# Optimization experiments

Measured on AMD Instinct MI355X. Metric: run time of the kernel, lower is better.

The kernel has to match this reference:

```python
import jax, jax.numpy as jnp
import numpy as np

B, P, CV = 2, 1024, 768
V, DNB, K = 50000, 300, 3
H = 768  # max(512, v_dim)
TOTAL_IN = CV + K * DNB + K  # include_scores=True
EPS = 1e-12


def setup_inputs() -> dict:
    key = jax.random.key(0)
    ks = jax.random.split(key, 7)
    v_seq = jax.random.normal(ks[0], (B, P, CV), dtype=jnp.float32)
    T = jax.random.normal(ks[1], (V, CV), dtype=jnp.float32)
    T_clip = T / jnp.linalg.norm(T, axis=-1, keepdims=True)  # bank rows are L2-normalized
    nb_vecs = jax.random.normal(ks[2], (V, DNB), dtype=jnp.float32)
    W1 = jax.random.normal(ks[3], (TOTAL_IN, H), dtype=jnp.float32) * (1.0 / np.sqrt(TOTAL_IN))
    b1 = jnp.zeros((H,), dtype=jnp.float32)
    W2 = jax.random.normal(ks[4], (H, CV), dtype=jnp.float32) * (1.0 / np.sqrt(H))
    b2 = jnp.zeros((CV,), dtype=jnp.float32)
    return {"v_seq": v_seq, "T_clip": T_clip, "nb_vecs": nb_vecs,
            "W1": W1, "b1": b1, "W2": W2, "b2": b2}


def _layer_norm(x, eps=1e-5):
    mu = jnp.mean(x, axis=-1, keepdims=True)
    var = jnp.var(x, axis=-1, keepdims=True)
    return (x - mu) * jax.lax.rsqrt(var + eps)


def reference(v_seq, T_clip, nb_vecs, W1, b1, W2, b2):
    # --- retrieve (no_grad in original) ---
    q = v_seq / jnp.maximum(jnp.linalg.norm(v_seq, axis=-1, keepdims=True), EPS)
    S = jnp.einsum('bpc,vc->bpv', q, T_clip)            # (B,P,V) cosine sims
    val, idx = jax.lax.top_k(S, K)                       # (B,P,K) each
    nb_sel = nb_vecs[idx]                                # gather -> (B,P,K,DNB)
    # --- fuse_concat ---
    nb_flat = nb_sel.reshape(B, P, K * DNB)
    combined = jnp.concatenate([v_seq, nb_flat, val], axis=-1)  # (B,P,TOTAL_IN)
    h = jax.nn.gelu(combined @ W1 + b1, approximate=False)      # nn.GELU default = erf
    fused = h @ W2 + b2                                          # dropout inactive (eval)
    return _layer_norm(fused)                                    # F.layer_norm, no affine
```

## Files before the change

### kernel.cpp

```cpp
#include <hip/hip_runtime.h>
#include <hip/hip_bf16.h>

typedef unsigned short u16;
typedef unsigned int u32;
typedef __attribute__((ext_vector_type(4))) unsigned short u16x4;
typedef __attribute__((ext_vector_type(8))) unsigned short u16x8;
typedef __attribute__((ext_vector_type(8))) short bf16x8;
typedef __attribute__((ext_vector_type(4))) float f32x4;

#define ROWS 2048
#define CV 768
#define VOCAB 50000
#define NPAD 50176
#define NTILES 196
#define NSEG 392
#define NSEGP 392
#define DNB 300
#define TOTAL_IN 1671
#define KPAD1 1696
#define HD 768
#define NT 12

__device__ __forceinline__ u16 f2bf(float f) {
  union { __hip_bfloat16 h; u16 u; } x;
  x.h = __float2bfloat16(f);
  return x.u;
}

__device__ __forceinline__ u16 bfkey(u16 u) {
  return (u & 0x8000) ? (u16)~u : (u16)(u | 0x8000);
}

__device__ __forceinline__ void gload16(const u16* g, const u16* l) {
  __builtin_amdgcn_global_load_lds(
      (const __attribute__((address_space(1))) void*)g,
      (__attribute__((address_space(3))) void*)l, 16, 0, 0);
}

__device__ __forceinline__ float block_sum256(float v, float* ws) {
#pragma unroll
  for (int off = 32; off > 0; off >>= 1) v += __shfl_xor(v, off, 64);
  int tid = threadIdx.x;
  if ((tid & 63) == 0) ws[tid >> 6] = v;
  __syncthreads();
  float s = ws[0] + ws[1] + ws[2] + ws[3];
  __syncthreads();
  return s;
}

__global__ __launch_bounds__(256) void normalize_kernel(
    const float* __restrict__ v_seq, float* __restrict__ rinv, u16* __restrict__ q16) {
  __shared__ float ws[4];
  int row = blockIdx.x, tid = threadIdx.x;
  const float* x = v_seq + (size_t)row * CV;
  float x0 = x[tid], x1 = x[tid + 256], x2 = x[tid + 512];
  float s = block_sum256(x0 * x0 + x1 * x1 + x2 * x2, ws);
  float denom = fmaxf(sqrtf(s), 1e-12f);
  float inv = 1.0f / denom;
  u16* qb = q16 + (size_t)row * CV;
  qb[tid] = f2bf(x0 * inv); qb[tid + 256] = f2bf(x1 * inv); qb[tid + 512] = f2bf(x2 * inv);
  if (tid == 0) rinv[row] = inv;
}

__global__ __launch_bounds__(256) void cvt_bf16_kernel(
    const float* __restrict__ src, u16* __restrict__ dst, int n4) {
  int i = blockIdx.x * 256 + threadIdx.x;
  int stride = gridDim.x * 256;
  for (; i < n4; i += stride) {
    float4 v = reinterpret_cast<const float4*>(src)[i];
    u16x4 o = {f2bf(v.x), f2bf(v.y), f2bf(v.z), f2bf(v.w)};
    reinterpret_cast<u16x4*>(dst)[i] = o;
  }
}

__global__ __launch_bounds__(256) void transpose_cvt_kernel(
    const float* __restrict__ src, u16* __restrict__ dst, int Ksrc, int ldk, int N) {
  __shared__ float tile[32][33];
  int tx = threadIdx.x & 31, ty = threadIdx.x >> 5;
  int kb = blockIdx.x * 32, nb = blockIdx.y * 32;
#pragma unroll
  for (int i = 0; i < 4; ++i) {
    int k = kb + ty + i * 8, n = nb + tx;
    tile[ty + i * 8][tx] = (k < Ksrc) ? src[(size_t)k * N + n] : 0.f;
  }
  __syncthreads();
#pragma unroll
  for (int i = 0; i < 4; ++i) {
    int n = nb + ty + i * 8, k = kb + tx;
    dst[(size_t)n * ldk + k] = f2bf(tile[tx][ty + i * 8]);
  }
}

__global__ __launch_bounds__(512, 2) void score_gemm_256(
    const u16* __restrict__ q16, const u16* __restrict__ T16,
    u16* __restrict__ S16, u16* __restrict__ segmax) {
  __shared__ __align__(16) u16 lds[65536];
  __shared__ float smx[256][4];

  int tid = threadIdx.x;
  int w = tid >> 6, lane = tid & 63;
  int wr = w >> 2, wc = w & 3;
  int l15 = lane & 15, l4 = lane >> 4;

  int bid = blockIdx.x;
  int wg = (bid & 7) * NTILES + (bid >> 3);
  int mtile = wg & 7, ntile = wg >> 3;
  int m0 = mtile * 256, n0 = ntile * 256;

  int t8 = tid >> 3;
  int jcol = (((tid & 7) ^ (t8 & 7)) << 3);
  int rowA = m0 + t8;
  int rowB0 = n0 + t8;        rowB0 = rowB0 > (VOCAB - 1) ? (VOCAB - 1) : rowB0;
  int rowB1 = n0 + 64 + t8;   rowB1 = rowB1 > (VOCAB - 1) ? (VOCAB - 1) : rowB1;
  int rowB2 = n0 + 128 + t8;  rowB2 = rowB2 > (VOCAB - 1) ? (VOCAB - 1) : rowB2;
  int rowB3 = n0 + 192 + t8;  rowB3 = rowB3 > (VOCAB - 1) ? (VOCAB - 1) : rowB3;
  int w512 = w * 512;

  int xorv = (l15 & 7) << 4;
  int l416 = l4 << 4;
  int c0 = ((l416) ^ xorv) >> 1;
  int c1 = ((64 + l416) ^ xorv) >> 1;
  int aro = (wr * 128 + l15) * 64;
  int bro = 16384 + (wc * 64 + l15) * 64;

  f32x4 acc[8][4];
#pragma unroll
  for (int i = 0; i < 8; ++i)
#pragma unroll
    for (int j = 0; j < 4; ++j) acc[i][j] = {0.f, 0.f, 0.f, 0.f};

  bf16x8 af[2][4], bfr[2][4];

#define STAGE_A(R0) gload16(q16 + (size_t)(rowA + (R0)) * CV + ktn + jcol, \
                            &lds[nbase + (R0) * 64 + w512])
#define STAGE_B0() gload16(T16 + (size_t)rowB0 * CV + ktn + jcol, &lds[nbase + 16384 + w512])
#define STAGE_B1() gload16(T16 + (size_t)rowB1 * CV + ktn + jcol, &lds[nbase + 16384 + 4096 + w512])
#define STAGE_B2() gload16(T16 + (size_t)rowB2 * CV + ktn + jcol, &lds[nbase + 16384 + 8192 + w512])
#define STAGE_B3() gload16(T16 + (size_t)rowB3 * CV + ktn + jcol, &lds[nbase + 16384 + 12288 + w512])

#define LDA4(MIB)                                                           \
  _Pragma("unroll") for (int ks = 0; ks < 2; ++ks)                          \
  _Pragma("unroll") for (int mi = 0; mi < 4; ++mi)                          \
    af[ks][mi] = *reinterpret_cast<const bf16x8*>(                          \
        &lds[cbase + aro + ((MIB) + mi) * 1024 + (ks ? c1 : c0)]);

#define LDB2(NIB)                                                           \
  _Pragma("unroll") for (int ks = 0; ks < 2; ++ks)                          \
  _Pragma("unroll") for (int ni = 0; ni < 2; ++ni)                          \
    bfr[ks][(NIB) + ni] = *reinterpret_cast<const bf16x8*>(                 \
        &lds[cbase + bro + ((NIB) + ni) * 1024 + (ks ? c1 : c0)]);

#define MFMAQ(MIB, NIB)                                                     \
  _Pragma("unroll") for (int mi = 0; mi < 4; ++mi)                          \
  _Pragma("unroll") for (int ni = 0; ni < 2; ++ni) {                        \
    acc[(MIB) + mi][(NIB) + ni] = __builtin_amdgcn_mfma_f32_16x16x32_bf16(  \
        af[0][mi], bfr[0][(NIB) + ni], acc[(MIB) + mi][(NIB) + ni], 0, 0, 0); \
    acc[(MIB) + mi][(NIB) + ni] = __builtin_amdgcn_mfma_f32_16x16x32_bf16(  \
        af[1][mi], bfr[1][(NIB) + ni], acc[(MIB) + mi][(NIB) + ni], 0, 0, 0); \
  }

  {
    int nbase = 0, ktn = 0;
    STAGE_B0(); STAGE_B1(); STAGE_B2(); STAGE_B3();
    STAGE_A(0); STAGE_A(128); STAGE_A(64); STAGE_A(192);
  }

  for (int t = 0; t < NT; ++t) {
    int cb = t & 1;
    int cbase = cb * 32768;
    int nbase = cbase ^ 32768;
    int ktn = ((t + 1 < NT) ? (t + 1) : t) * 64;

    asm volatile("s_waitcnt vmcnt(2)" ::: "memory");
    __builtin_amdgcn_s_barrier();

    LDA4(0)
    LDB2(0)
    STAGE_B0(); STAGE_B1();
    __builtin_amdgcn_s_barrier();
    __builtin_amdgcn_s_setprio(1);
    MFMAQ(0, 0)
    __builtin_amdgcn_s_setprio(0);
    __builtin_amdgcn_s_barrier();

    LDB2(2)
    STAGE_B2(); STAGE_B3();
    __builtin_amdgcn_s_barrier();
    __builtin_amdgcn_s_setprio(1);
    MFMAQ(0, 2)
    __builtin_amdgcn_s_setprio(0);
    asm volatile("s_waitcnt vmcnt(4)" ::: "memory");
    __builtin_amdgcn_s_barrier();

    LDA4(4)
    STAGE_A(0); STAGE_A(128);
    __builtin_amdgcn_s_barrier();
    __builtin_amdgcn_s_setprio(1);
    MFMAQ(4, 0)
    __builtin_amdgcn_s_setprio(0);
    __builtin_amdgcn_s_barrier();

    STAGE_A(64); STAGE_A(192);
    __builtin_amdgcn_s_setprio(1);
    MFMAQ(4, 2)
    __builtin_amdgcn_s_setprio(0);
  }
  asm volatile("s_waitcnt vmcnt(0)" ::: "memory");
  __builtin_amdgcn_s_barrier();

#pragma unroll
  for (int mi = 0; mi < 8; ++mi)
#pragma unroll
    for (int ni = 0; ni < 4; ++ni) {
      int gr = m0 + wr * 128 + mi * 16 + l4 * 4;
      int gc = n0 + wc * 64 + ni * 16 + l15;
#pragma unroll
      for (int r = 0; r < 4; ++r)
        S16[(size_t)(gr + r) * NPAD + gc] = f2bf(acc[mi][ni][r]);
    }

#pragma unroll
  for (int mi = 0; mi < 8; ++mi)
#pragma unroll
    for (int r = 0; r < 4; ++r) {
      float v = -3e38f;
#pragma unroll
      for (int ni = 0; ni < 4; ++ni) {
        bool ok = (n0 + wc * 64 + ni * 16 + l15) < VOCAB;
        v = fmaxf(v, ok ? acc[mi][ni][r] : -3e38f);
      }
#pragma unroll
      for (int d = 1; d < 16; d <<= 1) v = fmaxf(v, __shfl_xor(v, d, 64));
      if (l15 == 0) smx[wr * 128 + mi * 16 + l4 * 4 + r][wc] = v;
    }
  __syncthreads();
  if (tid < 256) {
    float s0 = fmaxf(smx[tid][0], smx[tid][1]);
    float s1 = fmaxf(smx[tid][2], smx[tid][3]);
    segmax[(size_t)(m0 + tid) * NSEGP + 2 * ntile]     = bfkey(f2bf(s0));
    segmax[(size_t)(m0 + tid) * NSEGP + 2 * ntile + 1] = bfkey(f2bf(s1));
  }
#undef STAGE_A
#undef STAGE_B0
#undef STAGE_B1
#undef STAGE_B2
#undef STAGE_B3
#undef LDA4
#undef LDB2
#undef MFMAQ
}

template <int ACT, int OUTBF>
__global__ __launch_bounds__(256) void gemm_bt(
    const u16* __restrict__ A, int lda,
    const u16* __restrict__ B, int ldb, int nclamp,
    int Kdim, const float* __restrict__ bias,
    float* __restrict__ Cf, u16* __restrict__ Cb, int ldc) {
  __shared__ __align__(16) u16 Asm[128 * 32];
  __shared__ __align__(16) u16 Bsm[128 * 32];
  int tid = threadIdx.x;
  int w = tid >> 6, lane = tid & 63;
  int wr = w >> 1, wc = w & 1;
  int m0 = blockIdx.x * 128;
  int n0 = blockIdx.y * 128;
  f32x4 acc[4][4];
#pragma unroll
  for (int i = 0; i < 4; ++i)
#pragma unroll
    for (int j = 0; j < 4; ++j) acc[i][j] = {0.f, 0.f, 0.f, 0.f};

  int r0 = tid >> 2, s0 = tid & 3;
  int b0r = n0 + r0;       b0r = b0r > nclamp ? nclamp : b0r;
  int b1r = n0 + 64 + r0;  b1r = b1r > nclamp ? nclamp : b1r;

  for (int k0 = 0; k0 < Kdim; k0 += 32) {
    __syncthreads();
    gload16(A + (size_t)(m0 + r0) * lda + k0 + s0 * 8, Asm + w * 512);
    gload16(A + (size_t)(m0 + 64 + r0) * lda + k0 + s0 * 8, Asm + 2048 + w * 512);
    gload16(B + (size_t)b0r * ldb + k0 + s0 * 8, Bsm + w * 512);
    gload16(B + (size_t)b1r * ldb + k0 + s0 * 8, Bsm + 2048 + w * 512);
    __syncthreads();
    int l15 = lane & 15, l4 = lane >> 4;
    bf16x8 af[4], bfr[4];
#pragma unroll
    for (int mi = 0; mi < 4; ++mi)
      af[mi] = *reinterpret_cast<const bf16x8*>(Asm + (wr * 64 + mi * 16 + l15) * 32 + l4 * 8);
#pragma unroll
    for (int ni = 0; ni < 4; ++ni)
      bfr[ni] = *reinterpret_cast<const bf16x8*>(Bsm + (wc * 64 + ni * 16 + l15) * 32 + l4 * 8);
#pragma unroll
    for (int mi = 0; mi < 4; ++mi)
#pragma unroll
      for (int ni = 0; ni < 4; ++ni)
        acc[mi][ni] = __builtin_amdgcn_mfma_f32_16x16x32_bf16(af[mi], bfr[ni], acc[mi][ni], 0, 0, 0);
  }

  int l15 = lane & 15, l4 = lane >> 4;
#pragma unroll
  for (int mi = 0; mi < 4; ++mi) {
#pragma unroll
    for (int ni = 0; ni < 4; ++ni) {
      int gr = m0 + wr * 64 + mi * 16 + l4 * 4;
      int gc = n0 + wc * 64 + ni * 16 + l15;
      float bv = bias ? bias[gc] : 0.f;
#pragma unroll
      for (int r = 0; r < 4; ++r) {
        float x = acc[mi][ni][r] + bv;
        if (ACT) x = 0.5f * x * (1.0f + erff(x * 0.70710678118654752f));
        size_t co = (size_t)(gr + r) * ldc + gc;
        if (OUTBF) Cb[co] = f2bf(x);
        else       Cf[co] = x;
      }
    }
  }
}

__global__ __launch_bounds__(256) void segsel_topk(
    const u16* __restrict__ segmax, const u16* __restrict__ S,
    int* __restrict__ cidx) {
  __shared__ u32 skey[448];
  __shared__ u32 winners[16];
  __shared__ u32 cl[256][16];
  int row = blockIdx.x, tid = threadIdx.x;

  if (tid < 224) {
#pragma unroll
    for (int j = 0; j < 2; ++j) {
      int s = tid * 2 + j;
      u32 k = 0;
      if (s < NSEG) k = ((u32)segmax[(size_t)row * NSEGP + s] << 9) | (u32)(511 - s);
      skey[s] = k;
    }
  }
  __syncthreads();

  if (tid < 64) {
    u32 v[7];
#pragma unroll
    for (int j = 0; j < 7; ++j) v[j] = skey[tid + 64 * j];
#pragma unroll
    for (int rd = 0; rd < 16; ++rd) {
      u32 m = v[0];
#pragma unroll
      for (int j = 1; j < 7; ++j) m = (v[j] > m) ? v[j] : m;
#pragma unroll
      for (int d = 1; d < 64; d <<= 1) {
        u32 o = (u32)__shfl_xor((int)m, d, 64);
        m = (o > m) ? o : m;
      }
#pragma unroll
      for (int j = 0; j < 7; ++j) v[j] = (v[j] == m) ? 0u : v[j];
      if (tid == 0) winners[rd] = m;
    }
  }
  __syncthreads();

  int wi = tid >> 4, off = (tid & 15) * 8;
  int seg = 511 - (int)(winners[wi] & 511);
  const u16* Sr = S + (size_t)row * NPAD + seg * 128 + off;
  u16x8 vv = *reinterpret_cast<const u16x8*>(Sr);
  u32 ck[8];
  int gbase = seg * 128 + off;
#pragma unroll
  for (int jj = 0; jj < 8; ++jj) {
    int g = gbase + jj;
    u32 c = ((u32)bfkey(vv[jj]) << 16) | (u32)(0xFFFF - g);
    ck[jj] = (g >= VOCAB) ? 0u : c;
  }
#define CE(i, j) { u32 a = ck[i], b = ck[j]; ck[i] = a > b ? a : b; ck[j] = a > b ? b : a; }
  CE(0,1) CE(2,3) CE(4,5) CE(6,7)
  CE(0,2) CE(1,3) CE(4,6) CE(5,7)
  CE(1,2) CE(5,6)
  CE(0,4) CE(1,5) CE(2,6) CE(3,7)
  CE(2,4) CE(3,5)
  CE(1,2) CE(3,4) CE(5,6)
#undef CE
#pragma unroll
  for (int k = 0; k < 8; ++k) cl[tid][k] = ck[k];
#pragma unroll
  for (int k = 8; k < 16; ++k) cl[tid][k] = 0u;
  __syncthreads();

  for (int s = 128; s >= 1; s >>= 1) {
    if (tid < s) {
      u32 ov[16];
      int pa = 0, pb = 0;
#pragma unroll
      for (int k = 0; k < 16; ++k) {
        u32 va = cl[tid][pa], vb = cl[tid + s][pb];
        bool ta = va >= vb;
        ov[k] = ta ? va : vb;
        pa += ta ? 1 : 0;
        pb += ta ? 0 : 1;
      }
#pragma unroll
      for (int k = 0; k < 16; ++k) cl[tid][k] = ov[k];
    }
    __syncthreads();
  }
  if (tid < 16) cidx[(size_t)row * 16 + tid] = 0xFFFF - (int)(cl[0][tid] & 0xFFFF);
}

__global__ __launch_bounds__(256) void rescore_concat(
    const float* __restrict__ v_seq, const float* __restrict__ rinv,
    const float* __restrict__ T, const int* __restrict__ cidx,
    const float* __restrict__ nb, u16* __restrict__ c16) {
  __shared__ float sex[16];
  __shared__ float sval[3];
  __shared__ int sidx[3];
  int row = blockIdx.x, tid = threadIdx.x;
  int wv = tid >> 6, lane = tid & 63;
  const float* __restrict__ qr = v_seq + (size_t)row * CV;
  float ri = rinv[row];
#pragma unroll
  for (int c0 = 0; c0 < 4; ++c0) {
    int c = wv + c0 * 4;
    int n = cidx[(size_t)row * 16 + c];
    const float* tr = T + (size_t)n * CV;
    float part = 0.f;
    int kb = lane * 12;
#pragma unroll
    for (int j3 = 0; j3 < 3; ++j3) {
      float4 a = *reinterpret_cast<const float4*>(tr + kb + j3 * 4);
      float4 b = *reinterpret_cast<const float4*>(qr + kb + j3 * 4);
      part += a.x * b.x + a.y * b.y + a.z * b.z + a.w * b.w;
    }
#pragma unroll
    for (int off = 32; off >= 1; off >>= 1) part += __shfl_xor(part, off, 64);
    if (lane == 0) sex[c] = part * ri;
  }
  __syncthreads();
  if (tid == 0) {
    float xv[16]; int xi[16];
#pragma unroll
    for (int c = 0; c < 16; ++c) { xv[c] = sex[c]; xi[c] = cidx[(size_t)row * 16 + c]; }
    for (int t = 0; t < 3; ++t) {
      float bv = -__builtin_inff(); int bi = 0x7fffffff, bc = -1;
#pragma unroll
      for (int c = 0; c < 16; ++c) {
        if (xi[c] < 0) continue;
        if (xv[c] > bv || (xv[c] == bv && xi[c] < bi)) { bv = xv[c]; bi = xi[c]; bc = c; }
      }
      sval[t] = bv; sidx[t] = bi;
      xi[bc] = -1;
    }
  }
  __syncthreads();

  u16* c = c16 + (size_t)row * KPAD1;
  if (tid < 192) {
    float4 v = *reinterpret_cast<const float4*>(qr + tid * 4);
    u16x4 o = {f2bf(v.x), f2bf(v.y), f2bf(v.z), f2bf(v.w)};
    *reinterpret_cast<u16x4*>(c + tid * 4) = o;
  }
  int i0 = sidx[0], i1 = sidx[1], i2 = sidx[2];
  if (tid < 75) {
    float4 v = *reinterpret_cast<const float4*>(nb + (size_t)i0 * DNB + tid * 4);
    u16x4 o = {f2bf(v.x), f2bf(v.y), f2bf(v.z), f2bf(v.w)};
    *reinterpret_cast<u16x4*>(c + CV + tid * 4) = o;
    v = *reinterpret_cast<const float4*>(nb + (size_t)i1 * DNB + tid * 4);
    o = {f2bf(v.x), f2bf(v.y), f2bf(v.z), f2bf(v.w)};
    *reinterpret_cast<u16x4*>(c + CV + DNB + tid * 4) = o;
    v = *reinterpret_cast<const float4*>(nb + (size_t)i2 * DNB + tid * 4);
    o = {f2bf(v.x), f2bf(v.y), f2bf(v.z), f2bf(v.w)};
    *reinterpret_cast<u16x4*>(c + CV + 2 * DNB + tid * 4) = o;
  }
  if (tid < 28) {
    int o = CV + 3 * DNB + tid;
    c[o] = (tid < 3) ? f2bf(sval[tid]) : (u16)0;
  }
}

__global__ __launch_bounds__(256) void layernorm_kernel(float* __restrict__ C) {
  __shared__ float ws[4];
  int row = blockIdx.x, tid = threadIdx.x;
  float* x = C + (size_t)row * CV;
  float x0 = x[tid], x1 = x[tid + 256], x2 = x[tid + 512];
  float mu = block_sum256(x0 + x1 + x2, ws) * (1.0f / 768.0f);
  float d0 = x0 - mu, d1 = x1 - mu, d2 = x2 - mu;
  float var = block_sum256(d0 * d0 + d1 * d1 + d2 * d2, ws) * (1.0f / 768.0f);
  float inv = 1.0f / sqrtf(var + 1e-5f);
  x[tid] = d0 * inv; x[tid + 256] = d1 * inv; x[tid + 512] = d2 * inv;
}

extern "C" void kernel_launch(void* const* d_in, const int* in_sizes, int n_in,
                              void* d_out, int out_size, void* d_ws, size_t ws_size,
                              hipStream_t stream) {
  const float* v_seq = (const float*)d_in[0];
  const float* T = (const float*)d_in[1];
  const float* nb = (const float*)d_in[2];
  const float* W1 = (const float*)d_in[3];
  const float* b1 = (const float*)d_in[4];
  const float* W2 = (const float*)d_in[5];
  const float* b2 = (const float*)d_in[6];
  float* out = (float*)d_out;

  char* base = (char*)d_ws;
  size_t off = 0;
  auto alloc = [&](size_t bytes) -> void* {
    void* p = base + off;
    off += (bytes + 255) & ~(size_t)255;
    return p;
  };
  float* rinv = (float*)alloc((size_t)ROWS * 4);
  u16* q16   = (u16*)alloc((size_t)ROWS * CV * 2);
  u16* T16   = (u16*)alloc((size_t)VOCAB * CV * 2);
  u16* c16   = (u16*)alloc((size_t)ROWS * KPAD1 * 2);
  u16* h16   = (u16*)alloc((size_t)ROWS * HD * 2);
  u16* W1T   = (u16*)alloc((size_t)HD * KPAD1 * 2);
  u16* W2T   = (u16*)alloc((size_t)HD * HD * 2);
  u16* segmaxb = (u16*)alloc((size_t)ROWS * NSEGP * 2);
  int* cidx  = (int*)alloc((size_t)ROWS * 16 * 4);
  u16* S16   = (u16*)alloc((size_t)ROWS * NPAD * 2);

  normalize_kernel<<<ROWS, 256, 0, stream>>>(v_seq, rinv, q16);
  cvt_bf16_kernel<<<2048, 256, 0, stream>>>(T, T16, VOCAB * CV / 4);
  transpose_cvt_kernel<<<dim3(KPAD1 / 32, HD / 32), 256, 0, stream>>>(W1, W1T, TOTAL_IN, KPAD1, HD);
  transpose_cvt_kernel<<<dim3(HD / 32, HD / 32), 256, 0, stream>>>(W2, W2T, HD, HD, HD);

  score_gemm_256<<<8 * NTILES, 512, 0, stream>>>(q16, T16, S16, segmaxb);
  segsel_topk<<<ROWS, 256, 0, stream>>>(segmaxb, S16, cidx);
  rescore_concat<<<ROWS, 256, 0, stream>>>(v_seq, rinv, T, cidx, nb, c16);
  gemm_bt<1, 1><<<dim3(ROWS / 128, HD / 128), 256, 0, stream>>>(
      c16, KPAD1, W1T, KPAD1, HD - 1, KPAD1, b1, nullptr, h16, HD);
  gemm_bt<0, 0><<<dim3(ROWS / 128, HD / 128), 256, 0, stream>>>(
      h16, HD, W2T, HD, HD - 1, HD, b2, out, nullptr, HD);
  layernorm_kernel<<<ROWS, 256, 0, stream>>>(out);
}
```

Baseline: 444.1 us.

## Fuse prep kernels, merge top-k select with rescore, halve MLP GEMM M-tile

```diff
diff --git a/kernel.cpp b/kernel.cpp
--- a/kernel.cpp
+++ b/kernel.cpp
@@ -20,6 +20,9 @@
 #define KPAD1 1696
 #define HD 768
 #define NT 12
+#define CVT_BLOCKS 2048
+#define W1T_BLOCKS (53 * 24)
+#define W2T_BLOCKS (24 * 24)
 
 __device__ __forceinline__ u16 f2bf(float f) {
   union { __hip_bfloat16 h; u16 u; } x;
@@ -48,36 +51,10 @@
   return s;
 }
 
-__global__ __launch_bounds__(256) void normalize_kernel(
-    const float* __restrict__ v_seq, float* __restrict__ rinv, u16* __restrict__ q16) {
-  __shared__ float ws[4];
-  int row = blockIdx.x, tid = threadIdx.x;
-  const float* x = v_seq + (size_t)row * CV;
-  float x0 = x[tid], x1 = x[tid + 256], x2 = x[tid + 512];
-  float s = block_sum256(x0 * x0 + x1 * x1 + x2 * x2, ws);
-  float denom = fmaxf(sqrtf(s), 1e-12f);
-  float inv = 1.0f / denom;
-  u16* qb = q16 + (size_t)row * CV;
-  qb[tid] = f2bf(x0 * inv); qb[tid + 256] = f2bf(x1 * inv); qb[tid + 512] = f2bf(x2 * inv);
-  if (tid == 0) rinv[row] = inv;
-}
-
-__global__ __launch_bounds__(256) void cvt_bf16_kernel(
-    const float* __restrict__ src, u16* __restrict__ dst, int n4) {
-  int i = blockIdx.x * 256 + threadIdx.x;
-  int stride = gridDim.x * 256;
-  for (; i < n4; i += stride) {
-    float4 v = reinterpret_cast<const float4*>(src)[i];
-    u16x4 o = {f2bf(v.x), f2bf(v.y), f2bf(v.z), f2bf(v.w)};
-    reinterpret_cast<u16x4*>(dst)[i] = o;
-  }
-}
-
-__global__ __launch_bounds__(256) void transpose_cvt_kernel(
-    const float* __restrict__ src, u16* __restrict__ dst, int Ksrc, int ldk, int N) {
-  __shared__ float tile[32][33];
+__device__ __forceinline__ void transpose_tile(
+    const float* __restrict__ src, u16* __restrict__ dst,
+    int Ksrc, int ldk, int N, int kb, int nb, float (*tile)[33]) {
   int tx = threadIdx.x & 31, ty = threadIdx.x >> 5;
-  int kb = blockIdx.x * 32, nb = blockIdx.y * 32;
 #pragma unroll
   for (int i = 0; i < 4; ++i) {
     int k = kb + ty + i * 8, n = nb + tx;
@@ -88,6 +65,41 @@
   for (int i = 0; i < 4; ++i) {
     int n = nb + ty + i * 8, k = kb + tx;
     dst[(size_t)n * ldk + k] = f2bf(tile[tx][ty + i * 8]);
+  }
+}
+
+__global__ __launch_bounds__(256) void prep_kernel(
+    const float* __restrict__ v_seq, float* __restrict__ rinv, u16* __restrict__ q16,
+    const float* __restrict__ T, u16* __restrict__ T16,
+    const float* __restrict__ W1, u16* __restrict__ W1T,
+    const float* __restrict__ W2, u16* __restrict__ W2T) {
+  __shared__ float tile[32][33];
+  int b = blockIdx.x, tid = threadIdx.x;
+  if (b < ROWS) {
+    float* ws = &tile[0][0];
+    const float* x = v_seq + (size_t)b * CV;
+    float x0 = x[tid], x1 = x[tid + 256], x2 = x[tid + 512];
+    float s = block_sum256(x0 * x0 + x1 * x1 + x2 * x2, ws);
+    float denom = fmaxf(sqrtf(s), 1e-12f);
+    float inv = 1.0f / denom;
+    u16* qb = q16 + (size_t)b * CV;
+    qb[tid] = f2bf(x0 * inv); qb[tid + 256] = f2bf(x1 * inv); qb[tid + 512] = f2bf(x2 * inv);
+    if (tid == 0) rinv[b] = inv;
+  } else if (b < ROWS + CVT_BLOCKS) {
+    int i = (b - ROWS) * 256 + tid;
+    const int n4 = VOCAB * CV / 4;
+    const int stride = CVT_BLOCKS * 256;
+    for (; i < n4; i += stride) {
+      float4 v = reinterpret_cast<const float4*>(T)[i];
+      u16x4 o = {f2bf(v.x), f2bf(v.y), f2bf(v.z), f2bf(v.w)};
+      reinterpret_cast<u16x4*>(T16)[i] = o;
+    }
+  } else if (b < ROWS + CVT_BLOCKS + W1T_BLOCKS) {
+    int bb = b - ROWS - CVT_BLOCKS;
+    transpose_tile(W1, W1T, TOTAL_IN, KPAD1, HD, (bb % 53) * 32, (bb / 53) * 32, tile);
+  } else {
+    int bb = b - ROWS - CVT_BLOCKS - W1T_BLOCKS;
+    transpose_tile(W2, W2T, HD, HD, HD, (bb % 24) * 32, (bb / 24) * 32, tile);
   }
 }
 
@@ -251,21 +263,21 @@
 }
 
 template <int ACT, int OUTBF>
-__global__ __launch_bounds__(256) void gemm_bt(
+__global__ __launch_bounds__(256) void gemm_bt64(
     const u16* __restrict__ A, int lda,
     const u16* __restrict__ B, int ldb, int nclamp,
     int Kdim, const float* __restrict__ bias,
     float* __restrict__ Cf, u16* __restrict__ Cb, int ldc) {
-  __shared__ __align__(16) u16 Asm[128 * 32];
+  __shared__ __align__(16) u16 Asm[64 * 32];
   __shared__ __align__(16) u16 Bsm[128 * 32];
   int tid = threadIdx.x;
   int w = tid >> 6, lane = tid & 63;
   int wr = w >> 1, wc = w & 1;
-  int m0 = blockIdx.x * 128;
+  int m0 = blockIdx.x * 64;
   int n0 = blockIdx.y * 128;
-  f32x4 acc[4][4];
-#pragma unroll
-  for (int i = 0; i < 4; ++i)
+  f32x4 acc[2][4];
+#pragma unroll
+  for (int i = 0; i < 2; ++i)
 #pragma unroll
     for (int j = 0; j < 4; ++j) acc[i][j] = {0.f, 0.f, 0.f, 0.f};
 
@@ -276,20 +288,19 @@
   for (int k0 = 0; k0 < Kdim; k0 += 32) {
     __syncthreads();
     gload16(A + (size_t)(m0 + r0) * lda + k0 + s0 * 8, Asm + w * 512);
-    gload16(A + (size_t)(m0 + 64 + r0) * lda + k0 + s0 * 8, Asm + 2048 + w * 512);
     gload16(B + (size_t)b0r * ldb + k0 + s0 * 8, Bsm + w * 512);
     gload16(B + (size_t)b1r * ldb + k0 + s0 * 8, Bsm + 2048 + w * 512);
     __syncthreads();
     int l15 = lane & 15, l4 = lane >> 4;
-    bf16x8 af[4], bfr[4];
-#pragma unroll
-    for (int mi = 0; mi < 4; ++mi)
-      af[mi] = *reinterpret_cast<const bf16x8*>(Asm + (wr * 64 + mi * 16 + l15) * 32 + l4 * 8);
+    bf16x8 af[2], bfr[4];
+#pragma unroll
+    for (int mi = 0; mi < 2; ++mi)
+      af[mi] = *reinterpret_cast<const bf16x8*>(Asm + (wr * 32 + mi * 16 + l15) * 32 + l4 * 8);
 #pragma unroll
     for (int ni = 0; ni < 4; ++ni)
       bfr[ni] = *reinterpret_cast<const bf16x8*>(Bsm + (wc * 64 + ni * 16 + l15) * 32 + l4 * 8);
 #pragma unroll
-    for (int mi = 0; mi < 4; ++mi)
+    for (int mi = 0; mi < 2; ++mi)
 #pragma unroll
       for (int ni = 0; ni < 4; ++ni)
         acc[mi][ni] = __builtin_amdgcn_mfma_f32_16x16x32_bf16(af[mi], bfr[ni], acc[mi][ni], 0, 0, 0);
@@ -297,10 +308,10 @@
 
   int l15 = lane & 15, l4 = lane >> 4;
 #pragma unroll
-  for (int mi = 0; mi < 4; ++mi) {
+  for (int mi = 0; mi < 2; ++mi) {
 #pragma unroll
     for (int ni = 0; ni < 4; ++ni) {
-      int gr = m0 + wr * 64 + mi * 16 + l4 * 4;
+      int gr = m0 + wr * 32 + mi * 16 + l4 * 4;
       int gc = n0 + wc * 64 + ni * 16 + l15;
       float bv = bias ? bias[gc] : 0.f;
 #pragma unroll
@@ -315,12 +326,18 @@
   }
 }
 
-__global__ __launch_bounds__(256) void segsel_topk(
+__global__ __launch_bounds__(256) void select_kernel(
     const u16* __restrict__ segmax, const u16* __restrict__ S,
-    int* __restrict__ cidx) {
+    const float* __restrict__ v_seq, const float* __restrict__ rinv,
+    const float* __restrict__ T, const float* __restrict__ nb,
+    u16* __restrict__ c16) {
   __shared__ u32 skey[448];
   __shared__ u32 winners[16];
   __shared__ u32 cl[256][16];
+  __shared__ int scand[16];
+  __shared__ float sex[16];
+  __shared__ float sval[3];
+  __shared__ int sidx[3];
   int row = blockIdx.x, tid = threadIdx.x;
 
   if (tid < 224) {
@@ -398,24 +415,16 @@
     }
     __syncthreads();
   }
-  if (tid < 16) cidx[(size_t)row * 16 + tid] = 0xFFFF - (int)(cl[0][tid] & 0xFFFF);
-}
-
-__global__ __launch_bounds__(256) void rescore_concat(
-    const float* __restrict__ v_seq, const float* __restrict__ rinv,
-    const float* __restrict__ T, const int* __restrict__ cidx,
-    const float* __restrict__ nb, u16* __restrict__ c16) {
-  __shared__ float sex[16];
-  __shared__ float sval[3];
-  __shared__ int sidx[3];
-  int row = blockIdx.x, tid = threadIdx.x;
+  if (tid < 16) scand[tid] = 0xFFFF - (int)(cl[0][tid] & 0xFFFF);
+  __syncthreads();
+
   int wv = tid >> 6, lane = tid & 63;
   const float* __restrict__ qr = v_seq + (size_t)row * CV;
   float ri = rinv[row];
 #pragma unroll
   for (int c0 = 0; c0 < 4; ++c0) {
     int c = wv + c0 * 4;
-    int n = cidx[(size_t)row * 16 + c];
+    int n = scand[c];
     const float* tr = T + (size_t)n * CV;
     float part = 0.f;
     int kb = lane * 12;
@@ -426,14 +435,14 @@
       part += a.x * b.x + a.y * b.y + a.z * b.z + a.w * b.w;
     }
 #pragma unroll
-    for (int off = 32; off >= 1; off >>= 1) part += __shfl_xor(part, off, 64);
+    for (int off2 = 32; off2 >= 1; off2 >>= 1) part += __shfl_xor(part, off2, 64);
     if (lane == 0) sex[c] = part * ri;
   }
   __syncthreads();
   if (tid == 0) {
     float xv[16]; int xi[16];
 #pragma unroll
-    for (int c = 0; c < 16; ++c) { xv[c] = sex[c]; xi[c] = cidx[(size_t)row * 16 + c]; }
+    for (int c = 0; c < 16; ++c) { xv[c] = sex[c]; xi[c] = scand[c]; }
     for (int t = 0; t < 3; ++t) {
       float bv = -__builtin_inff(); int bi = 0x7fffffff, bc = -1;
 #pragma unroll
@@ -510,20 +519,15 @@
   u16* W1T   = (u16*)alloc((size_t)HD * KPAD1 * 2);
   u16* W2T   = (u16*)alloc((size_t)HD * HD * 2);
   u16* segmaxb = (u16*)alloc((size_t)ROWS * NSEGP * 2);
-  int* cidx  = (int*)alloc((size_t)ROWS * 16 * 4);
   u16* S16   = (u16*)alloc((size_t)ROWS * NPAD * 2);
 
-  normalize_kernel<<<ROWS, 256, 0, stream>>>(v_seq, rinv, q16);
-  cvt_bf16_kernel<<<2048, 256, 0, stream>>>(T, T16, VOCAB * CV / 4);
-  transpose_cvt_kernel<<<dim3(KPAD1 / 32, HD / 32), 256, 0, stream>>>(W1, W1T, TOTAL_IN, KPAD1, HD);
-  transpose_cvt_kernel<<<dim3(HD / 32, HD / 32), 256, 0, stream>>>(W2, W2T, HD, HD, HD);
-
+  prep_kernel<<<ROWS + CVT_BLOCKS + W1T_BLOCKS + W2T_BLOCKS, 256, 0, stream>>>(
+      v_seq, rinv, q16, T, T16, W1, W1T, W2, W2T);
   score_gemm_256<<<8 * NTILES, 512, 0, stream>>>(q16, T16, S16, segmaxb);
-  segsel_topk<<<ROWS, 256, 0, stream>>>(segmaxb, S16, cidx);
-  rescore_concat<<<ROWS, 256, 0, stream>>>(v_seq, rinv, T, cidx, nb, c16);
-  gemm_bt<1, 1><<<dim3(ROWS / 128, HD / 128), 256, 0, stream>>>(
+  select_kernel<<<ROWS, 256, 0, stream>>>(segmaxb, S16, v_seq, rinv, T, nb, c16);
+  gemm_bt64<1, 1><<<dim3(ROWS / 64, HD / 128), 256, 0, stream>>>(
       c16, KPAD1, W1T, KPAD1, HD - 1, KPAD1, b1, nullptr, h16, HD);
-  gemm_bt<0, 0><<<dim3(ROWS / 128, HD / 128), 256, 0, stream>>>(
+  gemm_bt64<0, 0><<<dim3(ROWS / 64, HD / 128), 256, 0, stream>>>(
       h16, HD, W2T, HD, HD - 1, HD, b2, out, nullptr, HD);
   layernorm_kernel<<<ROWS, 256, 0, stream>>>(out);
 }
```

Result: faster. 391.4 us (-11.9%).
